# Optimization experiments

Hardware: AMD Instinct MI355X
Metric: run time of the kernel (lower is better)

The kernel has to match this reference:

```python
import jax, jax.numpy as jnp
import numpy as np

STATE_DIM = 512
ACTION_FEAT_DIM = 64
HIDDEN = 256


def setup_inputs() -> dict:
    key = jax.random.key(0)
    ks = jax.random.split(key, 8)
    B, K = 256, 1000
    state_embed = jax.random.normal(ks[0], (B, STATE_DIM), dtype=jnp.float32)
    action_feats = jax.random.normal(ks[1], (B, K, ACTION_FEAT_DIM), dtype=jnp.float32)
    s = 0.05
    W1 = jax.random.normal(ks[2], (STATE_DIM + ACTION_FEAT_DIM, HIDDEN), dtype=jnp.float32) * s
    b1 = jnp.zeros((HIDDEN,), dtype=jnp.float32)
    W2 = jax.random.normal(ks[3], (HIDDEN, HIDDEN // 2), dtype=jnp.float32) * s
    b2 = jnp.zeros((HIDDEN // 2,), dtype=jnp.float32)
    W3 = jax.random.normal(ks[4], (HIDDEN // 2, 1), dtype=jnp.float32) * s
    b3 = jnp.zeros((1,), dtype=jnp.float32)
    return {"state_embed": state_embed, "action_feats": action_feats,
            "W1": W1, "b1": b1, "W2": W2, "b2": b2, "W3": W3, "b3": b3}


def reference(state_embed, action_feats, W1, b1, W2, b2, W3, b3):
    # Faithful math: concat([state broadcast to K, action_feats]) -> Linear/ReLU x2 -> Linear(1)
    # Efficient form: split W1 rows so state part is computed once per batch row.
    W1_s = W1[:STATE_DIM]            # [state_dim, hidden]
    W1_a = W1[STATE_DIM:]            # [action_feat_dim, hidden]
    h_state = state_embed @ W1_s     # [B, hidden]
    h = jax.nn.relu(jnp.einsum('bkf,fh->bkh', action_feats, W1_a) + h_state[:, None, :] + b1)
    h = jax.nn.relu(jnp.einsum('bkh,hg->bkg', h, W2) + b2)
    logits = (jnp.einsum('bkg,go->bko', h, W3) + b3)[..., 0]  # [B, K]
    return logits
```

## Files before the change

### kernel.cpp

```cpp
#include <hip/hip_runtime.h>

typedef _Float16 f16;
typedef f16 f16x4 __attribute__((ext_vector_type(4)));
typedef f16 f16x8 __attribute__((ext_vector_type(8)));
typedef float f32x4 __attribute__((ext_vector_type(4)));


#define AF_STRIDE 72
#define H1_STRIDE 264

__global__ __launch_bounds__(256) void prep_kernel(const float* __restrict__ W1,
                                                   const float* __restrict__ W2,
                                                   const float* __restrict__ state,
                                                   const float* __restrict__ b1,
                                                   f16* __restrict__ pw1at,
                                                   f16* __restrict__ pw2,
                                                   float* __restrict__ hstate) {
    __shared__ float srow[512];
    int blk = blockIdx.x;
    int tid = threadIdx.x;
    if (blk < 24) {
        int idx = blk * 256 + tid;
        int F = idx >> 6;
        int L = idx & 63;
        int q = L >> 4, c = L & 15;
        f16x8 v;
        if (F < 32) {
            int mt = F >> 1, kt = F & 1;
            #pragma unroll
            for (int j = 0; j < 8; ++j) {
                int f = kt * 32 + q * 8 + j;
                v[j] = (f16)W1[(size_t)(512 + f) * 256 + mt * 16 + c];
            }
            *(f16x8*)(pw1at + ((size_t)F * 64 + L) * 8) = v;
        } else {
            int F2 = F - 32;
            int nt = F2 >> 3, kt = F2 & 7;
            #pragma unroll
            for (int j = 0; j < 8; ++j) {
                int k = kt * 32 + q * 8 + j;
                v[j] = (f16)W2[(size_t)k * 128 + nt * 16 + c];
            }
            *(f16x8*)(pw2 + ((size_t)F2 * 64 + L) * 8) = v;
        }
    } else {
        int b = blk - 24;
        srow[tid] = state[(size_t)b * 512 + tid];
        srow[tid + 256] = state[(size_t)b * 512 + 256 + tid];
        __syncthreads();
        float a0 = 0.f, a1 = 0.f;
        #pragma unroll 8
        for (int f = 0; f < 512; f += 2) {
            a0 = fmaf(srow[f],     W1[(size_t)f * 256 + tid],       a0);
            a1 = fmaf(srow[f + 1], W1[(size_t)(f + 1) * 256 + tid], a1);
        }
        hstate[(size_t)b * 256 + tid] = a0 + a1 + b1[tid];
    }
}

__global__ __launch_bounds__(256, 3) void fused_kernel(const float* __restrict__ afeat,
                                                       const float* __restrict__ hstate,
                                                       const f16* __restrict__ pw1at,
                                                       const f16* __restrict__ pw2,
                                                       const float* __restrict__ b2,
                                                       const float* __restrict__ W3,
                                                       const float* __restrict__ b3,
                                                       float* __restrict__ out) {
    __shared__ f16 afs2[128 * AF_STRIDE];
    __shared__ f16 h1s[64 * H1_STRIDE];
    float* lds3 = (float*)afs2;

    int tid = threadIdx.x;
    int w = tid >> 6;
    int L = tid & 63;
    int q = L >> 4, c = L & 15;
    int r0g = blockIdx.x * 128;

    #pragma unroll
    for (int i = 0; i < 4; ++i) {
        int id = i * 256 + tid;
        int row = id >> 3, c32 = id & 7;
        const float* p = afeat + (size_t)(r0g + row) * 64 + c32 * 8;
        f32x4 lo = *(const f32x4*)p;
        f32x4 hi = *(const f32x4*)(p + 4);
        f16x8 v;
        v[0] = (f16)lo[0]; v[1] = (f16)lo[1]; v[2] = (f16)lo[2]; v[3] = (f16)lo[3];
        v[4] = (f16)hi[0]; v[5] = (f16)hi[1]; v[6] = (f16)hi[2]; v[7] = (f16)hi[3];
        *(f16x8*)(afs2 + row * AF_STRIDE + c32 * 8) = v;
    }

    float b3v = b3[0];
    float b2v[2], w3v[2];
    #pragma unroll
    for (int ntl = 0; ntl < 2; ++ntl) {
        int col = (w * 2 + ntl) * 16 + c;
        b2v[ntl] = b2[col];
        w3v[ntl] = W3[col];
    }
    __syncthreads();

    for (int t = 0; t < 2; ++t) {
        int r0 = r0g + t * 64;
        int b0i = r0 / 1000;
        int boundary = (b0i + 1) * 1000;
        int b1i = b0i < 255 ? b0i + 1 : 255;

        f16x8 a1f[4][2];
        #pragma unroll
        for (int i = 0; i < 4; ++i)
            #pragma unroll
            for (int kt = 0; kt < 2; ++kt)
                a1f[i][kt] = *(const f16x8*)(pw1at + ((size_t)((4 * w + i) * 2 + kt) * 64 + L) * 8);

        f16x8 bf[4][2];
        #pragma unroll
        for (int nt = 0; nt < 4; ++nt)
            #pragma unroll
            for (int kt = 0; kt < 2; ++kt)
                bf[nt][kt] = *(const f16x8*)(afs2 + (t * 64 + nt * 16 + c) * AF_STRIDE + kt * 32 + q * 8);

        #pragma unroll
        for (int i = 0; i < 4; ++i) {
            f32x4 acc[4];
            #pragma unroll
            for (int nt = 0; nt < 4; ++nt) {
                acc[nt] = (f32x4){0.f, 0.f, 0.f, 0.f};
                #pragma unroll
                for (int kt = 0; kt < 2; ++kt)
                    acc[nt] = __builtin_amdgcn_mfma_f32_16x16x32_f16(
                        a1f[i][kt], bf[nt][kt], acc[nt], 0, 0, 0);
            }
            int hbase = (4 * w + i) * 16 + q * 4;
            f32x4 hsA = *(const f32x4*)(hstate + (size_t)b0i * 256 + hbase);
            f32x4 hsB = *(const f32x4*)(hstate + (size_t)b1i * 256 + hbase);
            #pragma unroll
            for (int nt = 0; nt < 4; ++nt) {
                bool sel = (r0 + nt * 16 + c) >= boundary;
                f16x4 hv;
                #pragma unroll
                for (int reg = 0; reg < 4; ++reg) {
                    float v = acc[nt][reg] + (sel ? hsB[reg] : hsA[reg]);
                    v = v > 0.f ? v : 0.f;
                    hv[reg] = (f16)v;
                }
                *(f16x4*)(h1s + (nt * 16 + c) * H1_STRIDE + hbase) = hv;
            }
        }
        __syncthreads();

        f32x4 acc2[4][2];
        #pragma unroll
        for (int rb = 0; rb < 4; ++rb) {
            acc2[rb][0] = (f32x4){0.f, 0.f, 0.f, 0.f};
            acc2[rb][1] = (f32x4){0.f, 0.f, 0.f, 0.f};
        }
        #pragma unroll
        for (int kt = 0; kt < 8; ++kt) {
            f16x8 a2[4];
            #pragma unroll
            for (int rb = 0; rb < 4; ++rb)
                a2[rb] = *(const f16x8*)(h1s + (rb * 16 + c) * H1_STRIDE + kt * 32 + q * 8);
            #pragma unroll
            for (int ntl = 0; ntl < 2; ++ntl) {
                f16x8 bfr = *(const f16x8*)(pw2 + ((size_t)((w * 2 + ntl) * 8 + kt) * 64 + L) * 8);
                #pragma unroll
                for (int rb = 0; rb < 4; ++rb)
                    acc2[rb][ntl] = __builtin_amdgcn_mfma_f32_16x16x32_f16(
                        a2[rb], bfr, acc2[rb][ntl], 0, 0, 0);
            }
        }

        #pragma unroll
        for (int rb = 0; rb < 4; ++rb) {
            float pr[4];
            #pragma unroll
            for (int reg = 0; reg < 4; ++reg) {
                float v0 = acc2[rb][0][reg] + b2v[0]; v0 = v0 > 0.f ? v0 : 0.f;
                float v1 = acc2[rb][1][reg] + b2v[1]; v1 = v1 > 0.f ? v1 : 0.f;
                pr[reg] = fmaf(v0, w3v[0], v1 * w3v[1]);
            }
            float e0 = (c & 1) ? pr[0] : pr[1];
            float k0 = (c & 1) ? pr[1] : pr[0];
            float e1 = (c & 1) ? pr[2] : pr[3];
            float k1 = (c & 1) ? pr[3] : pr[2];
            float a0 = k0 + __shfl_xor(e0, 1);
            float a1 = k1 + __shfl_xor(e1, 1);
            float e2 = (c & 2) ? a0 : a1;
            float k2 = (c & 2) ? a1 : a0;
            float s  = k2 + __shfl_xor(e2, 2);
            s += __shfl_xor(s, 4);
            s += __shfl_xor(s, 8);
            if ((c & 12) == 0)
                lds3[(rb * 16 + q * 4 + (c & 3)) * 6 + w] = s;
        }
        __syncthreads();

        if (tid < 64) {
            const float* pm = lds3 + tid * 6;
            out[r0 + tid] = pm[0] + pm[1] + pm[2] + pm[3] + b3v;
        }
    }
}

extern "C" void kernel_launch(void* const* d_in, const int* in_sizes, int n_in,
                              void* d_out, int out_size, void* d_ws, size_t ws_size,
                              hipStream_t stream) {
    const float* state = (const float*)d_in[0];
    const float* afeat = (const float*)d_in[1];
    const float* W1    = (const float*)d_in[2];
    const float* b1    = (const float*)d_in[3];
    const float* W2    = (const float*)d_in[4];
    const float* b2    = (const float*)d_in[5];
    const float* W3    = (const float*)d_in[6];
    const float* b3    = (const float*)d_in[7];
    float* out = (float*)d_out;

    float* hstate = (float*)d_ws;
    f16* pw1at = (f16*)((char*)d_ws + 65536 * sizeof(float));
    f16* pw2   = pw1at + 16384;

    prep_kernel<<<280, 256, 0, stream>>>(W1, W2, state, b1, pw1at, pw2, hstate);
    fused_kernel<<<2000, 256, 0, stream>>>(afeat, hstate, pw1at, pw2, b2, W3, b3, out);
}
```

Baseline: 153.0 us.

## Double fused kernel block to 512 threads, splitting hidden columns across eight waves

The fused MLP kernel now runs 8 wavefronts per block instead of 4. Each wave computes half as many layer-1 hidden tiles and one layer-2 output tile instead of two. The final partial sums are reduced across 8 waves through a dedicated LDS buffer, read back as vector loads. This spreads the per-block work over more waves to raise parallelism and cut per-wave register pressure. In exchange there is more redundant B-fragment loading from LDS per wave and heavier barrier synchronisation.

```diff
diff --git a/kernel.cpp b/kernel.cpp
--- a/kernel.cpp
+++ b/kernel.cpp
@@ -58,7 +58,7 @@
     }
 }
 
-__global__ __launch_bounds__(256, 3) void fused_kernel(const float* __restrict__ afeat,
+__global__ __launch_bounds__(512, 2) void fused_kernel(const float* __restrict__ afeat,
                                                        const float* __restrict__ hstate,
                                                        const f16* __restrict__ pw1at,
                                                        const f16* __restrict__ pw2,
@@ -68,7 +68,7 @@
                                                        float* __restrict__ out) {
     __shared__ f16 afs2[128 * AF_STRIDE];
     __shared__ f16 h1s[64 * H1_STRIDE];
-    float* lds3 = (float*)afs2;
+    __shared__ float lds3[64 * 8];
 
     int tid = threadIdx.x;
     int w = tid >> 6;
@@ -77,8 +77,8 @@
     int r0g = blockIdx.x * 128;
 
     #pragma unroll
-    for (int i = 0; i < 4; ++i) {
-        int id = i * 256 + tid;
+    for (int i = 0; i < 2; ++i) {
+        int id = i * 512 + tid;
         int row = id >> 3, c32 = id & 7;
         const float* p = afeat + (size_t)(r0g + row) * 64 + c32 * 8;
         f32x4 lo = *(const f32x4*)p;
@@ -90,13 +90,8 @@
     }
 
     float b3v = b3[0];
-    float b2v[2], w3v[2];
-    #pragma unroll
-    for (int ntl = 0; ntl < 2; ++ntl) {
-        int col = (w * 2 + ntl) * 16 + c;
-        b2v[ntl] = b2[col];
-        w3v[ntl] = W3[col];
-    }
+    float b2v = b2[w * 16 + c];
+    float w3v = W3[w * 16 + c];
     __syncthreads();
 
     for (int t = 0; t < 2; ++t) {
@@ -105,12 +100,12 @@
         int boundary = (b0i + 1) * 1000;
         int b1i = b0i < 255 ? b0i + 1 : 255;
 
-        f16x8 a1f[4][2];
-        #pragma unroll
-        for (int i = 0; i < 4; ++i)
+        f16x8 a1f[2][2];
+        #pragma unroll
+        for (int i = 0; i < 2; ++i)
             #pragma unroll
             for (int kt = 0; kt < 2; ++kt)
-                a1f[i][kt] = *(const f16x8*)(pw1at + ((size_t)((4 * w + i) * 2 + kt) * 64 + L) * 8);
+                a1f[i][kt] = *(const f16x8*)(pw1at + ((size_t)((2 * w + i) * 2 + kt) * 64 + L) * 8);
 
         f16x8 bf[4][2];
         #pragma unroll
@@ -120,7 +115,7 @@
                 bf[nt][kt] = *(const f16x8*)(afs2 + (t * 64 + nt * 16 + c) * AF_STRIDE + kt * 32 + q * 8);
 
         #pragma unroll
-        for (int i = 0; i < 4; ++i) {
+        for (int i = 0; i < 2; ++i) {
             f32x4 acc[4];
             #pragma unroll
             for (int nt = 0; nt < 4; ++nt) {
@@ -130,7 +125,7 @@
                     acc[nt] = __builtin_amdgcn_mfma_f32_16x16x32_f16(
                         a1f[i][kt], bf[nt][kt], acc[nt], 0, 0, 0);
             }
-            int hbase = (4 * w + i) * 16 + q * 4;
+            int hbase = (2 * w + i) * 16 + q * 4;
             f32x4 hsA = *(const f32x4*)(hstate + (size_t)b0i * 256 + hbase);
             f32x4 hsB = *(const f32x4*)(hstate + (size_t)b1i * 256 + hbase);
             #pragma unroll
@@ -148,26 +143,19 @@
         }
         __syncthreads();
 
-        f32x4 acc2[4][2];
-        #pragma unroll
-        for (int rb = 0; rb < 4; ++rb) {
-            acc2[rb][0] = (f32x4){0.f, 0.f, 0.f, 0.f};
-            acc2[rb][1] = (f32x4){0.f, 0.f, 0.f, 0.f};
-        }
+        f32x4 acc2[4];
+        #pragma unroll
+        for (int rb = 0; rb < 4; ++rb) acc2[rb] = (f32x4){0.f, 0.f, 0.f, 0.f};
         #pragma unroll
         for (int kt = 0; kt < 8; ++kt) {
             f16x8 a2[4];
             #pragma unroll
             for (int rb = 0; rb < 4; ++rb)
                 a2[rb] = *(const f16x8*)(h1s + (rb * 16 + c) * H1_STRIDE + kt * 32 + q * 8);
-            #pragma unroll
-            for (int ntl = 0; ntl < 2; ++ntl) {
-                f16x8 bfr = *(const f16x8*)(pw2 + ((size_t)((w * 2 + ntl) * 8 + kt) * 64 + L) * 8);
-                #pragma unroll
-                for (int rb = 0; rb < 4; ++rb)
-                    acc2[rb][ntl] = __builtin_amdgcn_mfma_f32_16x16x32_f16(
-                        a2[rb], bfr, acc2[rb][ntl], 0, 0, 0);
-            }
+            f16x8 bfr = *(const f16x8*)(pw2 + ((size_t)(w * 8 + kt) * 64 + L) * 8);
+            #pragma unroll
+            for (int rb = 0; rb < 4; ++rb)
+                acc2[rb] = __builtin_amdgcn_mfma_f32_16x16x32_f16(a2[rb], bfr, acc2[rb], 0, 0, 0);
         }
 
         #pragma unroll
@@ -175,9 +163,9 @@
             float pr[4];
             #pragma unroll
             for (int reg = 0; reg < 4; ++reg) {
-                float v0 = acc2[rb][0][reg] + b2v[0]; v0 = v0 > 0.f ? v0 : 0.f;
-                float v1 = acc2[rb][1][reg] + b2v[1]; v1 = v1 > 0.f ? v1 : 0.f;
-                pr[reg] = fmaf(v0, w3v[0], v1 * w3v[1]);
+                float v0 = acc2[rb][reg] + b2v;
+                v0 = v0 > 0.f ? v0 : 0.f;
+                pr[reg] = v0 * w3v;
             }
             float e0 = (c & 1) ? pr[0] : pr[1];
             float k0 = (c & 1) ? pr[1] : pr[0];
@@ -191,13 +179,15 @@
             s += __shfl_xor(s, 4);
             s += __shfl_xor(s, 8);
             if ((c & 12) == 0)
-                lds3[(rb * 16 + q * 4 + (c & 3)) * 6 + w] = s;
+                lds3[(rb * 16 + q * 4 + (c & 3)) * 8 + w] = s;
         }
         __syncthreads();
 
         if (tid < 64) {
-            const float* pm = lds3 + tid * 6;
-            out[r0 + tid] = pm[0] + pm[1] + pm[2] + pm[3] + b3v;
+            const float* pm = lds3 + tid * 8;
+            f32x4 s0 = *(const f32x4*)pm;
+            f32x4 s1 = *(const f32x4*)(pm + 4);
+            out[r0 + tid] = s0[0] + s0[1] + s0[2] + s0[3] + s1[0] + s1[1] + s1[2] + s1[3] + b3v;
         }
     }
 }
@@ -220,5 +210,5 @@
     f16* pw2   = pw1at + 16384;
 
     prep_kernel<<<280, 256, 0, stream>>>(W1, W2, state, b1, pw1at, pw2, hstate);
-    fused_kernel<<<2000, 256, 0, stream>>>(afeat, hstate, pw1at, pw2, b2, W3, b3, out);
+    fused_kernel<<<2000, 512, 0, stream>>>(afeat, hstate, pw1at, pw2, b2, W3, b3, out);
 }
```

Measured after the change: 147.2 us. -3.8%, faster.

## Split fused MLP work across eight waves per block with 512 threads

Applied to the files above, without the earlier changes.

Doubles the block size to 512 threads and partitions waves into hidden-column groups and action-row groups, so each wave computes half as many row tiles in both GEMM stages. The final reduction buffer becomes a dedicated small shared array indexed by column group. This aims to raise wave-level parallelism and occupancy and shrink per-wave register pressure, at the cost of loading weight fragments redundantly across the two row groups and adding more threads contending at barriers.

```diff
diff --git a/kernel.cpp b/kernel.cpp
--- a/kernel.cpp
+++ b/kernel.cpp
@@ -58,7 +58,7 @@
     }
 }
 
-__global__ __launch_bounds__(256, 3) void fused_kernel(const float* __restrict__ afeat,
+__global__ __launch_bounds__(512, 2) void fused_kernel(const float* __restrict__ afeat,
                                                        const float* __restrict__ hstate,
                                                        const f16* __restrict__ pw1at,
                                                        const f16* __restrict__ pw2,
@@ -68,17 +68,19 @@
                                                        float* __restrict__ out) {
     __shared__ f16 afs2[128 * AF_STRIDE];
     __shared__ f16 h1s[64 * H1_STRIDE];
-    float* lds3 = (float*)afs2;
+    __shared__ float lds3[64 * 4];
 
     int tid = threadIdx.x;
     int w = tid >> 6;
     int L = tid & 63;
     int q = L >> 4, c = L & 15;
+    int grp = w >> 1;
+    int agrp = w & 1;
     int r0g = blockIdx.x * 128;
 
     #pragma unroll
-    for (int i = 0; i < 4; ++i) {
-        int id = i * 256 + tid;
+    for (int i = 0; i < 2; ++i) {
+        int id = i * 512 + tid;
         int row = id >> 3, c32 = id & 7;
         const float* p = afeat + (size_t)(r0g + row) * 64 + c32 * 8;
         f32x4 lo = *(const f32x4*)p;
@@ -93,7 +95,7 @@
     float b2v[2], w3v[2];
     #pragma unroll
     for (int ntl = 0; ntl < 2; ++ntl) {
-        int col = (w * 2 + ntl) * 16 + c;
+        int col = (grp * 2 + ntl) * 16 + c;
         b2v[ntl] = b2[col];
         w3v[ntl] = W3[col];
     }
@@ -105,73 +107,75 @@
         int boundary = (b0i + 1) * 1000;
         int b1i = b0i < 255 ? b0i + 1 : 255;
 
-        f16x8 a1f[4][2];
-        #pragma unroll
-        for (int i = 0; i < 4; ++i)
+        f16x8 bf[2][2];
+        #pragma unroll
+        for (int j = 0; j < 2; ++j)
             #pragma unroll
             for (int kt = 0; kt < 2; ++kt)
-                a1f[i][kt] = *(const f16x8*)(pw1at + ((size_t)((4 * w + i) * 2 + kt) * 64 + L) * 8);
-
-        f16x8 bf[4][2];
-        #pragma unroll
-        for (int nt = 0; nt < 4; ++nt)
+                bf[j][kt] = *(const f16x8*)(afs2 +
+                    (t * 64 + (agrp * 2 + j) * 16 + c) * AF_STRIDE + kt * 32 + q * 8);
+
+        #pragma unroll
+        for (int i = 0; i < 4; ++i) {
+            int mt = grp * 4 + i;
+            f16x8 a1f[2];
             #pragma unroll
             for (int kt = 0; kt < 2; ++kt)
-                bf[nt][kt] = *(const f16x8*)(afs2 + (t * 64 + nt * 16 + c) * AF_STRIDE + kt * 32 + q * 8);
-
-        #pragma unroll
-        for (int i = 0; i < 4; ++i) {
-            f32x4 acc[4];
-            #pragma unroll
-            for (int nt = 0; nt < 4; ++nt) {
-                acc[nt] = (f32x4){0.f, 0.f, 0.f, 0.f};
+                a1f[kt] = *(const f16x8*)(pw1at + ((size_t)(mt * 2 + kt) * 64 + L) * 8);
+            f32x4 acc[2];
+            #pragma unroll
+            for (int j = 0; j < 2; ++j) {
+                acc[j] = (f32x4){0.f, 0.f, 0.f, 0.f};
                 #pragma unroll
                 for (int kt = 0; kt < 2; ++kt)
-                    acc[nt] = __builtin_amdgcn_mfma_f32_16x16x32_f16(
-                        a1f[i][kt], bf[nt][kt], acc[nt], 0, 0, 0);
-            }
-            int hbase = (4 * w + i) * 16 + q * 4;
+                    acc[j] = __builtin_amdgcn_mfma_f32_16x16x32_f16(
+                        a1f[kt], bf[j][kt], acc[j], 0, 0, 0);
+            }
+            int hbase = mt * 16 + q * 4;
             f32x4 hsA = *(const f32x4*)(hstate + (size_t)b0i * 256 + hbase);
             f32x4 hsB = *(const f32x4*)(hstate + (size_t)b1i * 256 + hbase);
             #pragma unroll
-            for (int nt = 0; nt < 4; ++nt) {
-                bool sel = (r0 + nt * 16 + c) >= boundary;
+            for (int j = 0; j < 2; ++j) {
+                int arow = (agrp * 2 + j) * 16 + c;
+                bool sel = (r0 + arow) >= boundary;
                 f16x4 hv;
                 #pragma unroll
                 for (int reg = 0; reg < 4; ++reg) {
-                    float v = acc[nt][reg] + (sel ? hsB[reg] : hsA[reg]);
+                    float v = acc[j][reg] + (sel ? hsB[reg] : hsA[reg]);
                     v = v > 0.f ? v : 0.f;
                     hv[reg] = (f16)v;
                 }
-                *(f16x4*)(h1s + (nt * 16 + c) * H1_STRIDE + hbase) = hv;
+                *(f16x4*)(h1s + arow * H1_STRIDE + hbase) = hv;
             }
         }
         __syncthreads();
 
-        f32x4 acc2[4][2];
-        #pragma unroll
-        for (int rb = 0; rb < 4; ++rb) {
+        f32x4 acc2[2][2];
+        #pragma unroll
+        for (int rb = 0; rb < 2; ++rb) {
             acc2[rb][0] = (f32x4){0.f, 0.f, 0.f, 0.f};
             acc2[rb][1] = (f32x4){0.f, 0.f, 0.f, 0.f};
         }
         #pragma unroll
         for (int kt = 0; kt < 8; ++kt) {
-            f16x8 a2[4];
-            #pragma unroll
-            for (int rb = 0; rb < 4; ++rb)
-                a2[rb] = *(const f16x8*)(h1s + (rb * 16 + c) * H1_STRIDE + kt * 32 + q * 8);
+            f16x8 a2[2];
+            #pragma unroll
+            for (int rb = 0; rb < 2; ++rb)
+                a2[rb] = *(const f16x8*)(h1s +
+                    ((agrp * 2 + rb) * 16 + c) * H1_STRIDE + kt * 32 + q * 8);
             #pragma unroll
             for (int ntl = 0; ntl < 2; ++ntl) {
-                f16x8 bfr = *(const f16x8*)(pw2 + ((size_t)((w * 2 + ntl) * 8 + kt) * 64 + L) * 8);
+                f16x8 bfr = *(const f16x8*)(pw2 +
+                    ((size_t)((grp * 2 + ntl) * 8 + kt) * 64 + L) * 8);
                 #pragma unroll
-                for (int rb = 0; rb < 4; ++rb)
+                for (int rb = 0; rb < 2; ++rb)
                     acc2[rb][ntl] = __builtin_amdgcn_mfma_f32_16x16x32_f16(
                         a2[rb], bfr, acc2[rb][ntl], 0, 0, 0);
             }
         }
 
         #pragma unroll
-        for (int rb = 0; rb < 4; ++rb) {
+        for (int rb = 0; rb < 2; ++rb) {
             float pr[4];
             #pragma unroll
             for (int reg = 0; reg < 4; ++reg) {
@@ -190,13 +194,15 @@
             float s  = k2 + __shfl_xor(e2, 2);
             s += __shfl_xor(s, 4);
             s += __shfl_xor(s, 8);
-            if ((c & 12) == 0)
-                lds3[(rb * 16 + q * 4 + (c & 3)) * 6 + w] = s;
+            if ((c & 12) == 0) {
+                int m = (agrp * 2 + rb) * 16 + q * 4 + (c & 3);
+                lds3[m * 4 + grp] = s;
+            }
         }
         __syncthreads();
 
         if (tid < 64) {
-            const float* pm = lds3 + tid * 6;
+            f32x4 pm = *(const f32x4*)(lds3 + tid * 4);
             out[r0 + tid] = pm[0] + pm[1] + pm[2] + pm[3] + b3v;
         }
     }
@@ -220,5 +226,5 @@
     f16* pw2   = pw1at + 16384;
 
     prep_kernel<<<280, 256, 0, stream>>>(W1, W2, state, b1, pw1at, pw2, hstate);
-    fused_kernel<<<2000, 256, 0, stream>>>(afeat, hstate, pw1at, pw2, b2, W3, b3, out);
+    fused_kernel<<<2000, 512, 0, stream>>>(afeat, hstate, pw1at, pw2, b2, W3, b3, out);
 }
```

New measurement: 152.0 us. About the same (-0.6%).
